# Optimization experiments

Measured on AMD Instinct MI355X. Metric: run time of the kernel, lower is better.

The kernel has to match this reference:

```python
import jax, jax.numpy as jnp
import numpy as np

B, K, N, D, L = 16, 16, 1024, 256, 8
LN_EPS = 1e-5


def setup_inputs() -> dict:
    key = jax.random.key(0)
    ks = jax.random.split(key, 12)
    w = lambda k, sh: jax.random.normal(k, sh, jnp.float32) * 0.02
    return {
        "H": jax.random.normal(ks[0], (B, K, N, D), jnp.float32),
        "eps": jax.random.normal(ks[1], (B, L, D), jnp.float32),  # single Gaussian draw per batch
        "mu": jnp.zeros((1, L, D), jnp.float32),
        "log_sigma": jnp.full((1, L, D), -2.0, jnp.float32),
        "Wq": w(ks[2], (D, D)), "bq": jnp.zeros((D,), jnp.float32),
        "Wk": w(ks[3], (D, D)), "bk": jnp.zeros((D,), jnp.float32),
        "Wv": w(ks[4], (D, D)), "bv": jnp.zeros((D,), jnp.float32),
        "W_ih": w(ks[5], (3 * D, D)), "b_ih": jnp.zeros((3 * D,), jnp.float32),
        "W_hh": w(ks[6], (3 * D, D)), "b_hh": jnp.zeros((3 * D,), jnp.float32),
        "W1": w(ks[7], (D, D)), "b1": jnp.zeros((D,), jnp.float32),
        "W2": w(ks[8], (D, D)), "b2": jnp.zeros((D,), jnp.float32),
        "ln_g": jnp.ones((D,), jnp.float32), "ln_b": jnp.zeros((D,), jnp.float32),
    }


def reference(H, eps, mu, log_sigma, Wq, bq, Wk, bk, Wv, bv,
              W_ih, b_ih, W_hh, b_hh, W1, b1, W2, b2, ln_g, ln_b):
    d = H.shape[-1]
    scale = 1.0 / jnp.sqrt(jnp.asarray(d, H.dtype))
    slots0 = mu + jnp.exp(log_sigma) * eps  # [B,L,D]

    def step(slots, h_t):  # slots [B,L,D], h_t [B,N,D]
        Q = slots @ Wq.T + bq
        Kt = h_t @ Wk.T + bk
        V = h_t @ Wv.T + bv
        scores = jnp.einsum("bld,bnd->bln", Q, Kt) * scale
        attn = jnp.nan_to_num(jax.nn.softmax(scores, axis=-1))
        upd = jnp.einsum("bln,bnd->bld", attn, V)
        # torch.nn.GRUCell(input=upd, hidden=slots)
        gi = upd @ W_ih.T + b_ih
        gh = slots @ W_hh.T + b_hh
        ir, iz, inn = jnp.split(gi, 3, axis=-1)
        hr, hz, hn = jnp.split(gh, 3, axis=-1)
        r = jax.nn.sigmoid(ir + hr)
        z = jax.nn.sigmoid(iz + hz)
        n = jnp.tanh(inn + r * hn)
        s2 = (1.0 - z) * n + z * slots
        # FFN + residual + LayerNorm
        ffn = jnp.maximum(s2 @ W1.T + b1, 0.0) @ W2.T + b2
        x = s2 + ffn
        mean = x.mean(axis=-1, keepdims=True)
        var = x.var(axis=-1, keepdims=True)
        s3 = (x - mean) / jnp.sqrt(var + LN_EPS) * ln_g + ln_b
        return s3, (s3, attn)

    _, (S, Beta) = jax.lax.scan(step, slots0, jnp.swapaxes(H, 0, 1))
    return jnp.swapaxes(S, 0, 1), jnp.swapaxes(Beta, 0, 1)  # [B,K,L,D], [B,K,L,N]
```

## Files before the change

kernel.cpp:

```cpp
#include <hip/hip_runtime.h>
#include <math.h>


#define Bn 16
#define KK 16
#define Nn 1024
#define Dn 256
#define Ln 8

#define OFF_WQK   0
#define OFF_BQK   65536
#define OFF_WGIT  65792
#define OFF_BGI   262400
#define OFF_WHHT  263168
#define OFF_W1T   459776
#define OFF_W2T   525312
#define OFF_SLOTS 590848
#define OFF_QK    623616
#define OFF_PAV   656384
#define OFF_PDEN  1704960
#define OFF_PG    1709056

__device__ __forceinline__ float sigmoidf_(float x) { return 1.f / (1.f + __expf(-x)); }

__global__ __launch_bounds__(256) void p1_kernel(
    const float* __restrict__ Wq, const float* __restrict__ bq,
    const float* __restrict__ Wk, float* __restrict__ Wqk, float* __restrict__ bqk) {
  int w = blockIdx.x, tid = threadIdx.x;
  if (w < 256) {
    float acc = 0.f;
    for (int a = 0; a < 256; ++a) acc += Wq[a * 256 + w] * Wk[a * 256 + tid];
    Wqk[w * 256 + tid] = acc;
  } else {
    float acc = 0.f;
    for (int a = 0; a < 256; ++a) acc += bq[a] * Wk[a * 256 + tid];
    bqk[tid] = acc;
  }
}

__global__ __launch_bounds__(256) void p2_kernel(
    const float* __restrict__ Wih, const float* __restrict__ bih,
    const float* __restrict__ Wv, const float* __restrict__ bv,
    float* __restrict__ WgiT, float* __restrict__ bgi) {
  int d = blockIdx.x, tid = threadIdx.x;
  float a0 = 0.f, a1 = 0.f, a2 = 0.f;
  for (int c = 0; c < 256; ++c) {
    float wv = Wv[c * 256 + d];
    a0 += Wih[tid * 256 + c] * wv;
    a1 += Wih[(tid + 256) * 256 + c] * wv;
    a2 += Wih[(tid + 512) * 256 + c] * wv;
  }
  WgiT[d * 768 + tid] = a0;
  WgiT[d * 768 + 256 + tid] = a1;
  WgiT[d * 768 + 512 + tid] = a2;
  if (d < 3) {
    int jj = d * 256 + tid;
    float s = bih[jj];
    for (int c = 0; c < 256; ++c) s += Wih[jj * 256 + c] * bv[c];
    bgi[jj] = s;
  }
}

__global__ __launch_bounds__(256) void p3_kernel(
    const float* __restrict__ Whh, const float* __restrict__ W1,
    const float* __restrict__ W2, float* __restrict__ WhhT,
    float* __restrict__ W1T, float* __restrict__ W2T) {
  __shared__ float tile[32][33];
  int wg = blockIdx.x, tid = threadIdx.x;
  const float* in; float* out; int R, C, tr, tc;
  if (wg < 192)      { in = Whh; out = WhhT; R = 768; C = 256; wg -= 0;   tr = wg >> 3; tc = wg & 7; }
  else if (wg < 256) { in = W1;  out = W1T;  R = 256; C = 256; wg -= 192; tr = wg >> 3; tc = wg & 7; }
  else               { in = W2;  out = W2T;  R = 256; C = 256; wg -= 256; tr = wg >> 3; tc = wg & 7; }
  int r = tid >> 5, c = tid & 31;
#pragma unroll
  for (int k = 0; k < 4; ++k)
    tile[r + 8 * k][c] = in[(tr * 32 + r + 8 * k) * C + tc * 32 + c];
  __syncthreads();
#pragma unroll
  for (int k = 0; k < 4; ++k)
    out[(tc * 32 + r + 8 * k) * R + tr * 32 + c] = tile[c][r + 8 * k];
}

__global__ __launch_bounds__(256) void init_slots_kernel(
    const float* __restrict__ eps, const float* __restrict__ mu,
    const float* __restrict__ lsig, float* __restrict__ slots) {
  int idx = blockIdx.x * 256 + threadIdx.x;
  int r = idx & 2047;
  slots[idx] = mu[r] + expf(lsig[r]) * eps[idx];
}

__global__ __launch_bounds__(256) void qk0_kernel(
    const float* __restrict__ Wqk, const float* __restrict__ bqk,
    const float* __restrict__ slots, float* __restrict__ Qkout) {
  __shared__ float sl_s[2048];
  int j = blockIdx.x & 7, b = blockIdx.x >> 3, tid = threadIdx.x;
  for (int k = 0; k < 8; ++k) sl_s[tid + k * 256] = slots[b * 2048 + tid + k * 256];
  __syncthreads();
  int l = tid >> 5, ee = j * 32 + (tid & 31);
  float acc = bqk[ee];
  for (int d = 0; d < 256; ++d) acc += sl_s[l * 256 + d] * Wqk[d * 256 + ee];
  Qkout[b * 2048 + l * 256 + ee] = acc;
}

__global__ __launch_bounds__(256) void attn_kernel(
    const float* __restrict__ H, const float* __restrict__ Qk,
    float* __restrict__ beta_out, float* __restrict__ par_av,
    float* __restrict__ par_den, int t) {
  __shared__ float h_s[32 * 258];
  __shared__ float qk_s[Ln * Dn];
  __shared__ float e_s[256];
  __shared__ float red[256];
  int tile = blockIdx.x, b = blockIdx.y, tid = threadIdx.x;
#pragma unroll
  for (int k = 0; k < 8; ++k) qk_s[tid + k * 256] = Qk[b * 2048 + tid + k * 256];
  const float* Hbase = H + (((long)b * KK + t) * Nn + tile * 32) * Dn;
  const float4* src = (const float4*)Hbase;
#pragma unroll
  for (int k = 0; k < 8; ++k) {
    int idx4 = tid + k * 256;
    int r = idx4 >> 6, d4 = idx4 & 63;
    float4 v = src[idx4];
    float* dst = &h_s[r * 258 + d4 * 4];
    ((float2*)dst)[0] = make_float2(v.x, v.y);
    ((float2*)dst)[1] = make_float2(v.z, v.w);
  }
  __syncthreads();
  int l = tid >> 5, row = tid & 31;
  {
    const float2* hr2 = (const float2*)(&h_s[row * 258]);
    const float2* qr2 = (const float2*)(&qk_s[l * 256]);
    float acc = 0.f;
#pragma unroll 8
    for (int e = 0; e < 128; ++e) {
      float2 hv = hr2[e], qv = qr2[e];
      acc += hv.x * qv.x + hv.y * qv.y;
    }
    float ev = __expf(acc * 0.0625f);
    e_s[tid] = ev;
    red[tid] = ev;
    beta_out[(((long)b * KK + t) * Ln + l) * Nn + tile * 32 + row] = ev;
  }
  __syncthreads();
  if (tid < 8) {
    float s = 0.f;
    for (int i = 0; i < 32; ++i) s += red[tid * 32 + i];
    par_den[(b * 32 + tile) * 8 + tid] = s;
  }
  float av[8];
#pragma unroll
  for (int i = 0; i < 8; ++i) av[i] = 0.f;
  for (int rr = 0; rr < 32; ++rr) {
    float hv = h_s[rr * 258 + tid];
#pragma unroll
    for (int i = 0; i < 8; ++i) av[i] += e_s[i * 32 + rr] * hv;
  }
  long pbase = (long)(b * 32 + tile) * 2048;
#pragma unroll
  for (int i = 0; i < 8; ++i) par_av[pbase + i * 256 + tid] = av[i];
}

__global__ __launch_bounds__(1024) void gru_kernel(
    const float* __restrict__ WgiT, const float* __restrict__ WhhT,
    const float* __restrict__ par_av, const float* __restrict__ par_den,
    const float* __restrict__ slots, float* __restrict__ Beta,
    float* __restrict__ pg, int t) {
  __shared__ float w_s[16 * 768];
  __shared__ float rupd[8][128];
  __shared__ float upd_s[128];
  __shared__ float sl_s[128];
  __shared__ float den_s[8];
  int b = blockIdx.x >> 4, kc = blockIdx.x & 15;
  int tid = threadIdx.x;

  const float4* wsrc = (const float4*)(WgiT + kc * 12288);
  float4 wv0 = wsrc[tid], wv1 = wsrc[tid + 1024], wv2 = wsrc[tid + 2048];
  {
    int g = tid >> 7, le = tid & 127;
    int l = le >> 4, e = le & 15;
    float ps = 0.f;
    long base = ((long)(b * 32)) * 2048 + l * 256 + kc * 16 + e;
#pragma unroll
    for (int i = 0; i < 4; ++i) ps += par_av[base + (long)(g * 4 + i) * 2048];
    rupd[g][le] = ps;
  }
  if (tid < 256) {
    int ll = tid >> 5, tl = tid & 31;
    float dv = par_den[(b * 32 + tl) * 8 + ll];
#pragma unroll
    for (int m = 1; m < 32; m <<= 1) dv += __shfl_xor(dv, m);
    if (tl == 0) den_s[ll] = 1.f / dv;
  }
  if (tid < 128) sl_s[tid] = slots[b * 2048 + (tid >> 4) * 256 + kc * 16 + (tid & 15)];
  ((float4*)w_s)[tid] = wv0;
  ((float4*)w_s)[tid + 1024] = wv1;
  ((float4*)w_s)[tid + 2048] = wv2;
  __syncthreads();

  if (tid < 512) {
    int idx = kc * 512 + tid;
    Beta[(((long)b * KK + t) * Ln) * Nn + idx] *= den_s[idx >> 10];
  }
  if (tid < 128) {
    float s = 0.f;
#pragma unroll
    for (int g = 0; g < 8; ++g) s += rupd[g][tid];
    upd_s[tid] = s * den_s[tid >> 4];
  }
  __syncthreads();

  int l4 = tid >> 8, cb = tid & 255;
  long pb0 = ((long)(b * 16 + kc) * 8 + l4) * 1536;
  long pb1 = ((long)(b * 16 + kc) * 8 + l4 + 4) * 1536;
  {
    float a0 = 0.f, a1 = 0.f, a2 = 0.f, a3 = 0.f, a4 = 0.f, a5 = 0.f;
#pragma unroll
    for (int e = 0; e < 16; ++e) {
      float u0 = upd_s[l4 * 16 + e];
      float u1 = upd_s[(l4 + 4) * 16 + e];
      float w0 = w_s[e * 768 + cb];
      float w1 = w_s[e * 768 + 256 + cb];
      float w2 = w_s[e * 768 + 512 + cb];
      a0 += u0 * w0; a1 += u0 * w1; a2 += u0 * w2;
      a3 += u1 * w0; a4 += u1 * w1; a5 += u1 * w2;
    }
    pg[pb0 + cb] = a0; pg[pb0 + 256 + cb] = a1; pg[pb0 + 512 + cb] = a2;
    pg[pb1 + cb] = a3; pg[pb1 + 256 + cb] = a4; pg[pb1 + 512 + cb] = a5;
  }
  __syncthreads();
  {
    const float4* hsrc = (const float4*)(WhhT + kc * 12288);
    ((float4*)w_s)[tid] = hsrc[tid];
    ((float4*)w_s)[tid + 1024] = hsrc[tid + 1024];
    ((float4*)w_s)[tid + 2048] = hsrc[tid + 2048];
  }
  __syncthreads();
  {
    float a0 = 0.f, a1 = 0.f, a2 = 0.f, a3 = 0.f, a4 = 0.f, a5 = 0.f;
#pragma unroll
    for (int e = 0; e < 16; ++e) {
      float s0 = sl_s[l4 * 16 + e];
      float s1 = sl_s[(l4 + 4) * 16 + e];
      float w0 = w_s[e * 768 + cb];
      float w1 = w_s[e * 768 + 256 + cb];
      float w2 = w_s[e * 768 + 512 + cb];
      a0 += s0 * w0; a1 += s0 * w1; a2 += s0 * w2;
      a3 += s1 * w0; a4 += s1 * w1; a5 += s1 * w2;
    }
    pg[pb0 + 768 + cb] = a0; pg[pb0 + 1024 + cb] = a1; pg[pb0 + 1280 + cb] = a2;
    pg[pb1 + 768 + cb] = a3; pg[pb1 + 1024 + cb] = a4; pg[pb1 + 1280 + cb] = a5;
  }
}

__global__ __launch_bounds__(1024) void chain2_kernel(
    const float* __restrict__ pg, const float* __restrict__ bgi,
    const float* __restrict__ bhh,
    const float* __restrict__ W1T, const float* __restrict__ b1,
    const float* __restrict__ W2T, const float* __restrict__ b2,
    const float* __restrict__ Wqk, const float* __restrict__ bqk,
    const float* __restrict__ ln_g, const float* __restrict__ ln_b,
    float* __restrict__ slots, float* __restrict__ S, float* __restrict__ Qk,
    int t) {
  __shared__ float sl_s[256], s2_s[256], f_s[256], s3_s[256];
  __shared__ float red6[6][4][256];
  __shared__ float lnred[8];
  int b = blockIdx.x >> 3, l = blockIdx.x & 7;
  int tid = threadIdx.x, q = tid >> 8, c = tid & 255;

  if (tid < 256) sl_s[tid] = slots[b * 2048 + l * 256 + tid];
  {
    float ir = 0, iz = 0, in_ = 0, hr = 0, hz = 0, hn = 0;
#pragma unroll
    for (int j = 0; j < 4; ++j) {
      const float* p = pg + ((long)(b * 16 + q * 4 + j) * 8 + l) * 1536;
      ir += p[c];        iz += p[256 + c];   in_ += p[512 + c];
      hr += p[768 + c];  hz += p[1024 + c];  hn  += p[1280 + c];
    }
    red6[0][q][c] = ir; red6[1][q][c] = iz; red6[2][q][c] = in_;
    red6[3][q][c] = hr; red6[4][q][c] = hz; red6[5][q][c] = hn;
  }
  __syncthreads();
  if (q == 0) {
    float tir = red6[0][0][c] + red6[0][1][c] + red6[0][2][c] + red6[0][3][c] + bgi[c];
    float tiz = red6[1][0][c] + red6[1][1][c] + red6[1][2][c] + red6[1][3][c] + bgi[256 + c];
    float tin = red6[2][0][c] + red6[2][1][c] + red6[2][2][c] + red6[2][3][c] + bgi[512 + c];
    float thr = red6[3][0][c] + red6[3][1][c] + red6[3][2][c] + red6[3][3][c] + bhh[c];
    float thz = red6[4][0][c] + red6[4][1][c] + red6[4][2][c] + red6[4][3][c] + bhh[256 + c];
    float thn = red6[5][0][c] + red6[5][1][c] + red6[5][2][c] + red6[5][3][c] + bhh[512 + c];
    float r = sigmoidf_(tir + thr);
    float z = sigmoidf_(tiz + thz);
    float n = tanhf(tin + r * thn);
    s2_s[c] = (1.f - z) * n + z * sl_s[c];
  }
  __syncthreads();

  {
    float f = 0.f;
#pragma unroll 4
    for (int i = 0; i < 64; ++i) {
      int e = q * 64 + i;
      f += s2_s[e] * W1T[e * 256 + c];
    }
    red6[0][q][c] = f;
  }
  __syncthreads();
  if (q == 0)
    f_s[c] = fmaxf(red6[0][0][c] + red6[0][1][c] + red6[0][2][c] + red6[0][3][c] + b1[c], 0.f);
  __syncthreads();

  {
    float x = 0.f;
#pragma unroll 4
    for (int i = 0; i < 64; ++i) {
      int e = q * 64 + i;
      x += f_s[e] * W2T[e * 256 + c];
    }
    red6[1][q][c] = x;
  }
  __syncthreads();
  float xv = 0.f;
  if (q == 0) {
    xv = red6[1][0][c] + red6[1][1][c] + red6[1][2][c] + red6[1][3][c] + b2[c] + s2_s[c];
    float sr = xv, qr = xv * xv;
#pragma unroll
    for (int m = 1; m < 64; m <<= 1) {
      sr += __shfl_xor(sr, m);
      qr += __shfl_xor(qr, m);
    }
    if ((c & 63) == 0) { lnred[c >> 6] = sr; lnred[4 + (c >> 6)] = qr; }
  }
  __syncthreads();
  if (q == 0) {
    float m = (lnred[0] + lnred[1] + lnred[2] + lnred[3]) * (1.f / 256.f);
    float v = (lnred[4] + lnred[5] + lnred[6] + lnred[7]) * (1.f / 256.f) - m * m;
    float s3 = (xv - m) * rsqrtf(v + 1e-5f) * ln_g[c] + ln_b[c];
    s3_s[c] = s3;
    S[(((long)b * KK + t) * Ln + l) * Dn + c] = s3;
    slots[b * 2048 + l * 256 + c] = s3;
  }
  __syncthreads();

  {
    float qacc = 0.f;
#pragma unroll 4
    for (int i = 0; i < 64; ++i) {
      int e = q * 64 + i;
      qacc += s3_s[e] * Wqk[e * 256 + c];
    }
    red6[0][q][c] = qacc;
  }
  __syncthreads();
  if (q == 0)
    Qk[b * 2048 + l * 256 + c] =
        red6[0][0][c] + red6[0][1][c] + red6[0][2][c] + red6[0][3][c] + bqk[c];
}

extern "C" void kernel_launch(void* const* d_in, const int* in_sizes, int n_in,
                              void* d_out, int out_size, void* d_ws, size_t ws_size,
                              hipStream_t stream) {
  const float* H    = (const float*)d_in[0];
  const float* eps  = (const float*)d_in[1];
  const float* mu   = (const float*)d_in[2];
  const float* lsig = (const float*)d_in[3];
  const float* Wq   = (const float*)d_in[4];
  const float* bq   = (const float*)d_in[5];
  const float* Wk   = (const float*)d_in[6];
  const float* Wv   = (const float*)d_in[8];
  const float* bv   = (const float*)d_in[9];
  const float* Wih  = (const float*)d_in[10];
  const float* bih  = (const float*)d_in[11];
  const float* Whh  = (const float*)d_in[12];
  const float* bhh  = (const float*)d_in[13];
  const float* W1   = (const float*)d_in[14];
  const float* b1   = (const float*)d_in[15];
  const float* W2   = (const float*)d_in[16];
  const float* b2   = (const float*)d_in[17];
  const float* ln_g = (const float*)d_in[18];
  const float* ln_b = (const float*)d_in[19];

  float* out = (float*)d_out;
  float* S    = out;
  float* Beta = out + (long)Bn * KK * Ln * Dn;

  float* ws = (float*)d_ws;
  float* Wqk   = ws + OFF_WQK;
  float* bqk   = ws + OFF_BQK;
  float* WgiT  = ws + OFF_WGIT;
  float* bgi   = ws + OFF_BGI;
  float* WhhT  = ws + OFF_WHHT;
  float* W1T   = ws + OFF_W1T;
  float* W2T   = ws + OFF_W2T;
  float* slots = ws + OFF_SLOTS;
  float* Qk    = ws + OFF_QK;
  float* pav   = ws + OFF_PAV;
  float* pden  = ws + OFF_PDEN;
  float* pg    = ws + OFF_PG;

  p1_kernel<<<257, 256, 0, stream>>>(Wq, bq, Wk, Wqk, bqk);
  p2_kernel<<<256, 256, 0, stream>>>(Wih, bih, Wv, bv, WgiT, bgi);
  p3_kernel<<<320, 256, 0, stream>>>(Whh, W1, W2, WhhT, W1T, W2T);
  init_slots_kernel<<<128, 256, 0, stream>>>(eps, mu, lsig, slots);
  qk0_kernel<<<128, 256, 0, stream>>>(Wqk, bqk, slots, Qk);

  for (int t = 0; t < KK; ++t) {
    attn_kernel<<<dim3(32, 16), 256, 0, stream>>>(H, Qk, Beta, pav, pden, t);
    gru_kernel<<<256, 1024, 0, stream>>>(WgiT, WhhT, pav, pden, slots, Beta, pg, t);
    chain2_kernel<<<128, 1024, 0, stream>>>(pg, bgi, bhh, W1T, b1, W2T, b2,
                                            Wqk, bqk, ln_g, ln_b, slots, S, Qk, t);
  }
}
```

Baseline: 1.017 ms.

## Split FFN/LN chain into two wider kernels and defer Beta normalization

The per-step chain kernel is split into chain2a (GRU gates plus FFN, with the output columns split across two blocks) and chain2b (residual, LayerNorm and the next Qk projection, also split in halves). This doubles the block count from 128 to 256 so the latency-bound serial chain spreads over more CUs. Beta normalization moves out of the loop into one final kernel using stored denominators, and unroll pragmas are added to the setup kernels. In exchange it adds one extra launch per step plus workspace round-trips for the partial FFN outputs and s2, and some GRU gate work is done twice.

```diff
diff --git a/kernel.cpp b/kernel.cpp
--- a/kernel.cpp
+++ b/kernel.cpp
@@ -20,6 +20,9 @@
 #define OFF_PAV   656384
 #define OFF_PDEN  1704960
 #define OFF_PG    1709056
+#define OFF_PX    4854784
+#define OFF_DENS  4920320
+#define OFF_S2G   4922368
 
 __device__ __forceinline__ float sigmoidf_(float x) { return 1.f / (1.f + __expf(-x)); }
 
@@ -29,10 +32,12 @@
   int w = blockIdx.x, tid = threadIdx.x;
   if (w < 256) {
     float acc = 0.f;
+#pragma unroll 8
     for (int a = 0; a < 256; ++a) acc += Wq[a * 256 + w] * Wk[a * 256 + tid];
     Wqk[w * 256 + tid] = acc;
   } else {
     float acc = 0.f;
+#pragma unroll 8
     for (int a = 0; a < 256; ++a) acc += bq[a] * Wk[a * 256 + tid];
     bqk[tid] = acc;
   }
@@ -44,6 +49,7 @@
     float* __restrict__ WgiT, float* __restrict__ bgi) {
   int d = blockIdx.x, tid = threadIdx.x;
   float a0 = 0.f, a1 = 0.f, a2 = 0.f;
+#pragma unroll 4
   for (int c = 0; c < 256; ++c) {
     float wv = Wv[c * 256 + d];
     a0 += Wih[tid * 256 + c] * wv;
@@ -98,6 +104,7 @@
   __syncthreads();
   int l = tid >> 5, ee = j * 32 + (tid & 31);
   float acc = bqk[ee];
+#pragma unroll 8
   for (int d = 0; d < 256; ++d) acc += sl_s[l * 256 + d] * Wqk[d * 256 + ee];
   Qkout[b * 2048 + l * 256 + ee] = acc;
 }
@@ -162,14 +169,14 @@
 __global__ __launch_bounds__(1024) void gru_kernel(
     const float* __restrict__ WgiT, const float* __restrict__ WhhT,
     const float* __restrict__ par_av, const float* __restrict__ par_den,
-    const float* __restrict__ slots, float* __restrict__ Beta,
-    float* __restrict__ pg, int t) {
+    const float* __restrict__ slots, float* __restrict__ pg,
+    float* __restrict__ dens_all, int t) {
   __shared__ float w_s[16 * 768];
   __shared__ float rupd[8][128];
   __shared__ float upd_s[128];
   __shared__ float sl_s[128];
   __shared__ float den_s[8];
-  int b = blockIdx.x >> 4, kc = blockIdx.x & 15;
+  int b = blockIdx.x & 15, kc = blockIdx.x >> 4;
   int tid = threadIdx.x;
 
   const float4* wsrc = (const float4*)(WgiT + kc * 12288);
@@ -196,10 +203,7 @@
   ((float4*)w_s)[tid + 2048] = wv2;
   __syncthreads();
 
-  if (tid < 512) {
-    int idx = kc * 512 + tid;
-    Beta[(((long)b * KK + t) * Ln) * Nn + idx] *= den_s[idx >> 10];
-  }
+  if (kc == 0 && tid < 8) dens_all[(t * 16 + b) * 8 + tid] = den_s[tid];
   if (tid < 128) {
     float s = 0.f;
 #pragma unroll
@@ -251,107 +255,155 @@
   }
 }
 
-__global__ __launch_bounds__(1024) void chain2_kernel(
+__global__ __launch_bounds__(1024) void chain2a_kernel(
     const float* __restrict__ pg, const float* __restrict__ bgi,
     const float* __restrict__ bhh,
     const float* __restrict__ W1T, const float* __restrict__ b1,
-    const float* __restrict__ W2T, const float* __restrict__ b2,
+    const float* __restrict__ W2T,
+    const float* __restrict__ slots, float* __restrict__ s2g,
+    float* __restrict__ px) {
+  __shared__ float gsum[1536];
+  __shared__ float s2_s[256];
+  __shared__ float f1s[128];
+  __shared__ float red8[128 * 9];
+  __shared__ float red4[1024];
+  int wid = blockIdx.x;
+  int b = wid & 15, l = (wid >> 4) & 7, ph = wid >> 7;
+  int tid = threadIdx.x;
+
+  for (int col = tid; col < 1536; col += 1024) {
+    float v[16];
+#pragma unroll
+    for (int j = 0; j < 16; ++j) v[j] = pg[((long)(b * 16 + j) * 8 + l) * 1536 + col];
+    float a = 0.f;
+#pragma unroll
+    for (int j = 0; j < 16; ++j) a += v[j];
+    gsum[col] = a;
+  }
+  __syncthreads();
+  if (tid < 256) {
+    int c = tid;
+    float r = sigmoidf_(gsum[c] + bgi[c] + gsum[768 + c] + bhh[c]);
+    float z = sigmoidf_(gsum[256 + c] + bgi[256 + c] + gsum[1024 + c] + bhh[256 + c]);
+    float n = tanhf(gsum[512 + c] + bgi[512 + c] + r * (gsum[1280 + c] + bhh[512 + c]));
+    float s2 = (1.f - z) * n + z * slots[b * 2048 + l * 256 + c];
+    s2_s[c] = s2;
+    if (ph == 0) s2g[b * 2048 + l * 256 + c] = s2;
+  }
+  __syncthreads();
+  {
+    int kc = tid >> 7, h = tid & 127;
+    const float* wp = W1T + (kc * 32) * 256 + ph * 128 + h;
+    const float* sp = s2_s + kc * 32;
+    float acc = 0.f;
+#pragma unroll
+    for (int g = 0; g < 2; ++g) {
+      float w[16];
+#pragma unroll
+      for (int i = 0; i < 16; ++i) w[i] = wp[(g * 16 + i) * 256];
+#pragma unroll
+      for (int i = 0; i < 16; ++i) acc += sp[g * 16 + i] * w[i];
+    }
+    red8[h * 9 + kc] = acc;
+  }
+  __syncthreads();
+  if (tid < 128) {
+    float a = b1[ph * 128 + tid];
+#pragma unroll
+    for (int kc = 0; kc < 8; ++kc) a += red8[tid * 9 + kc];
+    f1s[tid] = fmaxf(a, 0.f);
+  }
+  __syncthreads();
+  {
+    int q = tid >> 8, c = tid & 255;
+    const float* wp = W2T + (ph * 128 + q * 32) * 256 + c;
+    const float* fp = f1s + q * 32;
+    float acc = 0.f;
+#pragma unroll
+    for (int g = 0; g < 2; ++g) {
+      float w[16];
+#pragma unroll
+      for (int i = 0; i < 16; ++i) w[i] = wp[(g * 16 + i) * 256];
+#pragma unroll
+      for (int i = 0; i < 16; ++i) acc += fp[g * 16 + i] * w[i];
+    }
+    red4[q * 256 + c] = acc;
+  }
+  __syncthreads();
+  if (tid < 256)
+    px[((long)(b * 8 + l) * 2 + ph) * 256 + tid] =
+        red4[tid] + red4[256 + tid] + red4[512 + tid] + red4[768 + tid];
+}
+
+__global__ __launch_bounds__(1024) void chain2b_kernel(
+    const float* __restrict__ px, const float* __restrict__ b2,
+    const float* __restrict__ ln_g, const float* __restrict__ ln_b,
     const float* __restrict__ Wqk, const float* __restrict__ bqk,
-    const float* __restrict__ ln_g, const float* __restrict__ ln_b,
-    float* __restrict__ slots, float* __restrict__ S, float* __restrict__ Qk,
-    int t) {
-  __shared__ float sl_s[256], s2_s[256], f_s[256], s3_s[256];
-  __shared__ float red6[6][4][256];
-  __shared__ float lnred[8];
-  int b = blockIdx.x >> 3, l = blockIdx.x & 7;
-  int tid = threadIdx.x, q = tid >> 8, c = tid & 255;
-
-  if (tid < 256) sl_s[tid] = slots[b * 2048 + l * 256 + tid];
-  {
-    float ir = 0, iz = 0, in_ = 0, hr = 0, hz = 0, hn = 0;
-#pragma unroll
-    for (int j = 0; j < 4; ++j) {
-      const float* p = pg + ((long)(b * 16 + q * 4 + j) * 8 + l) * 1536;
-      ir += p[c];        iz += p[256 + c];   in_ += p[512 + c];
-      hr += p[768 + c];  hz += p[1024 + c];  hn  += p[1280 + c];
-    }
-    red6[0][q][c] = ir; red6[1][q][c] = iz; red6[2][q][c] = in_;
-    red6[3][q][c] = hr; red6[4][q][c] = hz; red6[5][q][c] = hn;
-  }
-  __syncthreads();
-  if (q == 0) {
-    float tir = red6[0][0][c] + red6[0][1][c] + red6[0][2][c] + red6[0][3][c] + bgi[c];
-    float tiz = red6[1][0][c] + red6[1][1][c] + red6[1][2][c] + red6[1][3][c] + bgi[256 + c];
-    float tin = red6[2][0][c] + red6[2][1][c] + red6[2][2][c] + red6[2][3][c] + bgi[512 + c];
-    float thr = red6[3][0][c] + red6[3][1][c] + red6[3][2][c] + red6[3][3][c] + bhh[c];
-    float thz = red6[4][0][c] + red6[4][1][c] + red6[4][2][c] + red6[4][3][c] + bhh[256 + c];
-    float thn = red6[5][0][c] + red6[5][1][c] + red6[5][2][c] + red6[5][3][c] + bhh[512 + c];
-    float r = sigmoidf_(tir + thr);
-    float z = sigmoidf_(tiz + thz);
-    float n = tanhf(tin + r * thn);
-    s2_s[c] = (1.f - z) * n + z * sl_s[c];
-  }
-  __syncthreads();
-
-  {
-    float f = 0.f;
-#pragma unroll 4
-    for (int i = 0; i < 64; ++i) {
-      int e = q * 64 + i;
-      f += s2_s[e] * W1T[e * 256 + c];
-    }
-    red6[0][q][c] = f;
-  }
-  __syncthreads();
-  if (q == 0)
-    f_s[c] = fmaxf(red6[0][0][c] + red6[0][1][c] + red6[0][2][c] + red6[0][3][c] + b1[c], 0.f);
-  __syncthreads();
-
-  {
-    float x = 0.f;
-#pragma unroll 4
-    for (int i = 0; i < 64; ++i) {
-      int e = q * 64 + i;
-      x += f_s[e] * W2T[e * 256 + c];
-    }
-    red6[1][q][c] = x;
-  }
-  __syncthreads();
-  float xv = 0.f;
-  if (q == 0) {
-    xv = red6[1][0][c] + red6[1][1][c] + red6[1][2][c] + red6[1][3][c] + b2[c] + s2_s[c];
-    float sr = xv, qr = xv * xv;
-#pragma unroll
-    for (int m = 1; m < 64; m <<= 1) {
-      sr += __shfl_xor(sr, m);
-      qr += __shfl_xor(qr, m);
-    }
-    if ((c & 63) == 0) { lnred[c >> 6] = sr; lnred[4 + (c >> 6)] = qr; }
-  }
-  __syncthreads();
-  if (q == 0) {
-    float m = (lnred[0] + lnred[1] + lnred[2] + lnred[3]) * (1.f / 256.f);
-    float v = (lnred[4] + lnred[5] + lnred[6] + lnred[7]) * (1.f / 256.f) - m * m;
-    float s3 = (xv - m) * rsqrtf(v + 1e-5f) * ln_g[c] + ln_b[c];
-    s3_s[c] = s3;
-    S[(((long)b * KK + t) * Ln + l) * Dn + c] = s3;
-    slots[b * 2048 + l * 256 + c] = s3;
-  }
-  __syncthreads();
-
-  {
-    float qacc = 0.f;
-#pragma unroll 4
-    for (int i = 0; i < 64; ++i) {
-      int e = q * 64 + i;
-      qacc += s3_s[e] * Wqk[e * 256 + c];
-    }
-    red6[0][q][c] = qacc;
-  }
-  __syncthreads();
-  if (q == 0)
-    Qk[b * 2048 + l * 256 + c] =
-        red6[0][0][c] + red6[0][1][c] + red6[0][2][c] + red6[0][3][c] + bqk[c];
+    const float* __restrict__ s2g, float* __restrict__ slots,
+    float* __restrict__ S, float* __restrict__ QkG, int t) {
+  __shared__ float s3_s[256];
+  __shared__ float red8[128 * 9];
+  __shared__ float lnr[8];
+  int wid = blockIdx.x;
+  int b = wid & 15, l = (wid >> 4) & 7, ph = wid >> 7;
+  int tid = threadIdx.x;
+  if (tid < 256) {
+    long pb = (long)(b * 8 + l) * 2 * 256;
+    float x = px[pb + tid] + px[pb + 256 + tid] + b2[tid] + s2g[b * 2048 + l * 256 + tid];
+    s3_s[tid] = x;
+    float sr = x, qr = x * x;
+#pragma unroll
+    for (int m = 1; m < 64; m <<= 1) { sr += __shfl_xor(sr, m); qr += __shfl_xor(qr, m); }
+    if ((tid & 63) == 0) { lnr[tid >> 6] = sr; lnr[4 + (tid >> 6)] = qr; }
+  }
+  __syncthreads();
+  if (tid < 256) {
+    float m = (lnr[0] + lnr[1] + lnr[2] + lnr[3]) * (1.f / 256.f);
+    float v = (lnr[4] + lnr[5] + lnr[6] + lnr[7]) * (1.f / 256.f) - m * m;
+    float s3 = (s3_s[tid] - m) * rsqrtf(v + 1e-5f) * ln_g[tid] + ln_b[tid];
+    s3_s[tid] = s3;
+    if (ph == 0) {
+      S[(((long)(b * 16) + t) * 8 + l) * 256 + tid] = s3;
+      slots[b * 2048 + l * 256 + tid] = s3;
+    }
+  }
+  __syncthreads();
+  {
+    int kc = tid >> 7, c = tid & 127;
+    const float* wp = Wqk + (kc * 32) * 256 + ph * 128 + c;
+    const float* sp = s3_s + kc * 32;
+    float acc = 0.f;
+#pragma unroll
+    for (int g = 0; g < 2; ++g) {
+      float w[16];
+#pragma unroll
+      for (int i = 0; i < 16; ++i) w[i] = wp[(g * 16 + i) * 256];
+#pragma unroll
+      for (int i = 0; i < 16; ++i) acc += sp[g * 16 + i] * w[i];
+    }
+    red8[c * 9 + kc] = acc;
+  }
+  __syncthreads();
+  if (tid < 128) {
+    float a = bqk[ph * 128 + tid];
+#pragma unroll
+    for (int kc = 0; kc < 8; ++kc) a += red8[tid * 9 + kc];
+    QkG[b * 2048 + l * 256 + ph * 128 + tid] = a;
+  }
+}
+
+__global__ __launch_bounds__(1024) void beta_norm_kernel(
+    const float* __restrict__ dens_all, float* __restrict__ Beta) {
+  int wid = blockIdx.x;
+  int b = wid >> 4, t = wid & 15;
+  int tid = threadIdx.x;
+  long base = (((long)b * 16) + t) * 8192;
+#pragma unroll
+  for (int i = 0; i < 8; ++i) {
+    int idx = i * 1024 + tid;
+    int l = idx >> 10;
+    Beta[base + idx] *= dens_all[(t * 16 + b) * 8 + l];
+  }
 }
 
 extern "C" void kernel_launch(void* const* d_in, const int* in_sizes, int n_in,
@@ -394,6 +446,9 @@
   float* pav   = ws + OFF_PAV;
   float* pden  = ws + OFF_PDEN;
   float* pg    = ws + OFF_PG;
+  float* px    = ws + OFF_PX;
+  float* dens  = ws + OFF_DENS;
+  float* s2g   = ws + OFF_S2G;
 
   p1_kernel<<<257, 256, 0, stream>>>(Wq, bq, Wk, Wqk, bqk);
   p2_kernel<<<256, 256, 0, stream>>>(Wih, bih, Wv, bv, WgiT, bgi);
@@ -403,8 +458,10 @@
 
   for (int t = 0; t < KK; ++t) {
     attn_kernel<<<dim3(32, 16), 256, 0, stream>>>(H, Qk, Beta, pav, pden, t);
-    gru_kernel<<<256, 1024, 0, stream>>>(WgiT, WhhT, pav, pden, slots, Beta, pg, t);
-    chain2_kernel<<<128, 1024, 0, stream>>>(pg, bgi, bhh, W1T, b1, W2T, b2,
-                                            Wqk, bqk, ln_g, ln_b, slots, S, Qk, t);
-  }
-}
+    gru_kernel<<<256, 1024, 0, stream>>>(WgiT, WhhT, pav, pden, slots, pg, dens, t);
+    chain2a_kernel<<<256, 1024, 0, stream>>>(pg, bgi, bhh, W1T, b1, W2T, slots, s2g, px);
+    chain2b_kernel<<<256, 1024, 0, stream>>>(px, b2, ln_g, ln_b, Wqk, bqk,
+                                             s2g, slots, S, Qk, t);
+  }
+  beta_norm_kernel<<<256, 1024, 0, stream>>>(dens, Beta);
+}
```

Result: faster. 932.5 us (-8.3%).
